# Kernel tuning notes

Hardware: AMD Instinct MI355X
Metric: run time of the kernel (lower is better)

The kernel has to match this reference:

```python
import jax, jax.numpy as jnp
import numpy as np

ESP = 1e-10  # matches SRKNN.ESP
K = 16       # top-k neighbors


def _logmap(x):
    # sign-preserving log map (repo helper not shown; eps matches SRKNN.ESP)
    return jnp.sign(x) * jnp.log(jnp.abs(x) + ESP)


def setup_inputs() -> dict:
    key = jax.random.key(0)
    k1, k2, k3, k4 = jax.random.split(key, 4)
    B, C, H, W = 2, 128, 32, 32
    C2 = C // 2
    X = jax.random.normal(k1, (B, C, H, W), jnp.float32)
    # nn.Linear(C, C//2, bias=False) weights, torch layout [out, in]
    W_min = jax.random.normal(k2, (C2, C), jnp.float32) * 0.08
    W_sub = jax.random.normal(k3, (C2, C), jnp.float32) * 0.08
    M = jax.random.normal(k4, (C2, C2), jnp.float32)
    return {"X": X, "W_min": W_min, "W_sub": W_sub, "M": M}


def reference(X, W_min, W_sub, M):
    B, C, H, W = X.shape
    XV = jnp.transpose(X, (0, 2, 3, 1)).reshape(B, -1, C)  # [B, N, C]
    N = XV.shape[1]
    # project then log-map; pairwise (i=minuend, j=subtrahend) without repeat
    pm = _logmap(XV @ W_min.T)  # [B, N, C2]
    ps = _logmap(XV @ W_sub.T)  # [B, N, C2]
    subR = jax.nn.sigmoid(pm[:, :, None, :] - ps[:, None, :, :])  # [B, N, N, C2]
    A = M.T @ M  # [C2, C2] learned Mahalanobis metric
    dis = jnp.sqrt(jnp.sum(jnp.einsum('bijc,cd->bijd', subR, A) * subR, axis=-1))  # [B,N,N]
    diff = jax.nn.sigmoid(-dis)
    value, index = jax.lax.top_k(diff, K)  # [B, N, K]
    value = -value.reshape(B, -1, 1)       # [B, N*K, 1]
    index = index.reshape(B, -1)           # [B, N*K]
    return index, value
```

## Files before the change

### kernel.cpp

```cpp
#include <hip/hip_runtime.h>
#include <hip/hip_bf16.h>
#include <hip/hip_fp16.h>
#include <math.h>

#define NN 1024
#define CC 128
#define C2 64
#define KK 16
#define NCAND 24

#if __has_builtin(__builtin_amdgcn_exp2f)
#define EXP2F(x) __builtin_amdgcn_exp2f(x)
#else
#define EXP2F(x) exp2f(x)
#endif
#define LOG2E 1.4426950408889634f

typedef __fp16  hf2   __attribute__((ext_vector_type(2)));
typedef _Float16 half8 __attribute__((ext_vector_type(8)));
typedef float f32x4    __attribute__((ext_vector_type(4)));
typedef int   int4v    __attribute__((ext_vector_type(4)));
typedef unsigned int uint;

__device__ __forceinline__ float fast_rcp(float x) {
    return __builtin_amdgcn_rcpf(x);
}

#define LDS_FENCE() do { \
    asm volatile("s_waitcnt lgkmcnt(0)" ::: "memory"); \
    __builtin_amdgcn_sched_barrier(0); } while (0)

__global__ __launch_bounds__(128) void proj_buildA(
        const float* __restrict__ X,
        const float* __restrict__ Wm,
        const float* __restrict__ Ws,
        const float* __restrict__ M,
        float* __restrict__ pm,
        float* __restrict__ ps,
        float* __restrict__ psE,
        float* __restrict__ A) {
    if (blockIdx.x >= 2 * NN) {
        const int e = (blockIdx.x - 2 * NN) * 128 + threadIdx.x;
        const int c = e >> 6, d = e & 63;
        float acc = 0.f;
        #pragma unroll 8
        for (int r = 0; r < C2; ++r)
            acc = fmaf(M[r * C2 + c], M[r * C2 + d], acc);
        A[e] = acc;
        return;
    }

    const int bn = blockIdx.x;
    const int b  = bn >> 10;
    const int n  = bn & (NN - 1);
    const int t  = threadIdx.x;

    __shared__ float xv[CC];
    xv[t] = X[b * CC * NN + t * NN + n];
    __syncthreads();

    const int d = t & (C2 - 1);
    const float* wr = ((t < C2) ? Wm : Ws) + d * CC;
    float acc = 0.f;
    #pragma unroll
    for (int c = 0; c < CC; ++c)
        acc = fmaf(wr[c], xv[c], acc);

    float a = __fadd_rn(fabsf(acc), 1e-10f);
    float l = logf(a);
    float r = (acc > 0.f) ? l : ((acc < 0.f) ? -l : 0.f);
    if (t < C2) {
        pm[bn * C2 + d] = r;
    } else {
        ps[bn * C2 + d] = r;
        psE[bn * C2 + d] = EXP2F(r * LOG2E);
    }
}

#define SIGF16(PMEF, Y0, Y1, BF) do {                                         \
    float s0 = PMEF[0] * fast_rcp(PMEF[0] + (Y0).x);                          \
    float s1 = PMEF[1] * fast_rcp(PMEF[1] + (Y0).y);                          \
    float s2 = PMEF[2] * fast_rcp(PMEF[2] + (Y0).z);                          \
    float s3 = PMEF[3] * fast_rcp(PMEF[3] + (Y0).w);                          \
    float s4 = PMEF[4] * fast_rcp(PMEF[4] + (Y1).x);                          \
    float s5 = PMEF[5] * fast_rcp(PMEF[5] + (Y1).y);                          \
    float s6 = PMEF[6] * fast_rcp(PMEF[6] + (Y1).z);                          \
    float s7 = PMEF[7] * fast_rcp(PMEF[7] + (Y1).w);                          \
    hf2 p0 = __builtin_amdgcn_cvt_pkrtz(s0, s1);                              \
    hf2 p1 = __builtin_amdgcn_cvt_pkrtz(s2, s3);                              \
    hf2 p2 = __builtin_amdgcn_cvt_pkrtz(s4, s5);                              \
    hf2 p3 = __builtin_amdgcn_cvt_pkrtz(s6, s7);                              \
    int4v iv = { __builtin_bit_cast(int, p0), __builtin_bit_cast(int, p1),    \
                 __builtin_bit_cast(int, p2), __builtin_bit_cast(int, p3) };  \
    BF = __builtin_bit_cast(half8, iv);                                       \
} while (0)

#define MFMA4(AC, KT, B)                                                              \
    AC[0] = __builtin_amdgcn_mfma_f32_16x16x32_f16(af[0][KT], B, AC[0], 0, 0, 0);     \
    AC[1] = __builtin_amdgcn_mfma_f32_16x16x32_f16(af[1][KT], B, AC[1], 0, 0, 0);     \
    AC[2] = __builtin_amdgcn_mfma_f32_16x16x32_f16(af[2][KT], B, AC[2], 0, 0, 0);     \
    AC[3] = __builtin_amdgcn_mfma_f32_16x16x32_f16(af[3][KT], B, AC[3], 0, 0, 0);

#define STREAM(PMEF, T0, T1, T2, T3, AC) do {                                 \
    half8 b0, b1;                                                             \
    SIGF16(PMEF[0], T0, T1, b0);                                              \
    SIGF16(PMEF[1], T2, T3, b1);                                              \
    MFMA4(AC, 0, b0)                                                          \
    MFMA4(AC, 1, b1)                                                          \
} while (0)

__global__ __launch_bounds__(256, 2) void pair_topk(
        const float* __restrict__ pm,
        const float* __restrict__ ps,
        const float* __restrict__ psE,
        const float* __restrict__ Mf,
        const float* __restrict__ A,
        float* __restrict__ out) {
    const int tid  = threadIdx.x;
    const int wv   = tid >> 6;
    const int lane = tid & 63;
    const int g    = lane >> 4;
    const int lj   = lane & 15;
    const int rp   = wv >> 1;
    const int h    = wv & 1;

    const int rbase = blockIdx.x * 4;
    const int b     = rbase >> 10;

    __shared__ uint  d2u[4][NN];
    __shared__ float sC[4][C2];
    __shared__ float cdiffL[4][NCAND];

    const float* psb  = ps  + b * NN * C2;
    const float* psEb = psE + b * NN * C2;

    {
        const int r0 = rbase + rp * 2;

        float pmEf0[2][8], pmEf1[2][8];
        #pragma unroll
        for (int kt = 0; kt < 2; ++kt) {
            const float4 a0 = *(const float4*)(pm + r0 * C2 + kt * 32 + g * 8);
            const float4 a1 = *(const float4*)(pm + r0 * C2 + kt * 32 + g * 8 + 4);
            pmEf0[kt][0] = EXP2F(a0.x * LOG2E); pmEf0[kt][1] = EXP2F(a0.y * LOG2E);
            pmEf0[kt][2] = EXP2F(a0.z * LOG2E); pmEf0[kt][3] = EXP2F(a0.w * LOG2E);
            pmEf0[kt][4] = EXP2F(a1.x * LOG2E); pmEf0[kt][5] = EXP2F(a1.y * LOG2E);
            pmEf0[kt][6] = EXP2F(a1.z * LOG2E); pmEf0[kt][7] = EXP2F(a1.w * LOG2E);
            const float4 c0 = *(const float4*)(pm + (r0 + 1) * C2 + kt * 32 + g * 8);
            const float4 c1 = *(const float4*)(pm + (r0 + 1) * C2 + kt * 32 + g * 8 + 4);
            pmEf1[kt][0] = EXP2F(c0.x * LOG2E); pmEf1[kt][1] = EXP2F(c0.y * LOG2E);
            pmEf1[kt][2] = EXP2F(c0.z * LOG2E); pmEf1[kt][3] = EXP2F(c0.w * LOG2E);
            pmEf1[kt][4] = EXP2F(c1.x * LOG2E); pmEf1[kt][5] = EXP2F(c1.y * LOG2E);
            pmEf1[kt][6] = EXP2F(c1.z * LOG2E); pmEf1[kt][7] = EXP2F(c1.w * LOG2E);
        }

        half8 af[4][2];
        #pragma unroll
        for (int rt = 0; rt < 4; ++rt) {
            #pragma unroll
            for (int kt = 0; kt < 2; ++kt) {
                const float* mrow = Mf + (rt * 16 + lj) * C2 + kt * 32 + g * 8;
                const float4 m0 = *(const float4*)mrow;
                const float4 m1 = *(const float4*)(mrow + 4);
                float mv[8] = {m0.x, m0.y, m0.z, m0.w, m1.x, m1.y, m1.z, m1.w};
                #pragma unroll
                for (int e = 0; e < 8; ++e)
                    af[rt][kt][e] = (_Float16)mv[e];
            }
        }

        const int tbase = h * 32;
        const float* p0 = psEb + (long)((tbase + 0) * 16 + lj) * C2 + g * 8;
        const float* p1 = psEb + (long)((tbase + 1) * 16 + lj) * C2 + g * 8;
        float4 cA0 = *(const float4*)(p0);      float4 cA1 = *(const float4*)(p0 + 4);
        float4 cA2 = *(const float4*)(p0 + 32); float4 cA3 = *(const float4*)(p0 + 36);
        float4 cB0 = *(const float4*)(p1);      float4 cB1 = *(const float4*)(p1 + 4);
        float4 cB2 = *(const float4*)(p1 + 32); float4 cB3 = *(const float4*)(p1 + 36);

        #pragma unroll 1
        for (int it = 0; it < 16; ++it) {
            float4 nA0, nA1, nA2, nA3, nB0, nB1, nB2, nB3;
            if (it < 15) {
                const float* q0 = psEb + (long)((tbase + it * 2 + 2) * 16 + lj) * C2 + g * 8;
                const float* q1 = psEb + (long)((tbase + it * 2 + 3) * 16 + lj) * C2 + g * 8;
                nA0 = *(const float4*)(q0);      nA1 = *(const float4*)(q0 + 4);
                nA2 = *(const float4*)(q0 + 32); nA3 = *(const float4*)(q0 + 36);
                nB0 = *(const float4*)(q1);      nB1 = *(const float4*)(q1 + 4);
                nB2 = *(const float4*)(q1 + 32); nB3 = *(const float4*)(q1 + 36);
            }

            f32x4 a0A[4] = {{0,0,0,0},{0,0,0,0},{0,0,0,0},{0,0,0,0}};
            f32x4 a1A[4] = {{0,0,0,0},{0,0,0,0},{0,0,0,0},{0,0,0,0}};
            f32x4 a0B[4] = {{0,0,0,0},{0,0,0,0},{0,0,0,0},{0,0,0,0}};
            f32x4 a1B[4] = {{0,0,0,0},{0,0,0,0},{0,0,0,0},{0,0,0,0}};

            __builtin_amdgcn_s_setprio(1);
            STREAM(pmEf0, cA0, cA1, cA2, cA3, a0A);
            STREAM(pmEf1, cA0, cA1, cA2, cA3, a1A);
            STREAM(pmEf0, cB0, cB1, cB2, cB3, a0B);
            STREAM(pmEf1, cB0, cB1, cB2, cB3, a1B);
            __builtin_amdgcn_s_setprio(0);

            float s0A = 0.f, s1A = 0.f, s0B = 0.f, s1B = 0.f;
            #pragma unroll
            for (int e = 0; e < 4; ++e) {
                s0A = fmaf(a0A[0][e], a0A[0][e], s0A);
                s0A = fmaf(a0A[1][e], a0A[1][e], s0A);
                s0A = fmaf(a0A[2][e], a0A[2][e], s0A);
                s0A = fmaf(a0A[3][e], a0A[3][e], s0A);
                s1A = fmaf(a1A[0][e], a1A[0][e], s1A);
                s1A = fmaf(a1A[1][e], a1A[1][e], s1A);
                s1A = fmaf(a1A[2][e], a1A[2][e], s1A);
                s1A = fmaf(a1A[3][e], a1A[3][e], s1A);
                s0B = fmaf(a0B[0][e], a0B[0][e], s0B);
                s0B = fmaf(a0B[1][e], a0B[1][e], s0B);
                s0B = fmaf(a0B[2][e], a0B[2][e], s0B);
                s0B = fmaf(a0B[3][e], a0B[3][e], s0B);
                s1B = fmaf(a1B[0][e], a1B[0][e], s1B);
                s1B = fmaf(a1B[1][e], a1B[1][e], s1B);
                s1B = fmaf(a1B[2][e], a1B[2][e], s1B);
                s1B = fmaf(a1B[3][e], a1B[3][e], s1B);
            }
            s0A += __shfl_xor(s0A, 16, 64); s0A += __shfl_xor(s0A, 32, 64);
            s1A += __shfl_xor(s1A, 16, 64); s1A += __shfl_xor(s1A, 32, 64);
            s0B += __shfl_xor(s0B, 16, 64); s0B += __shfl_xor(s0B, 32, 64);
            s1B += __shfl_xor(s1B, 16, 64); s1B += __shfl_xor(s1B, 32, 64);
            if (lane < 16) {
                const int jA = (tbase + it * 2 + 0) * 16 + lane;
                const int jB = (tbase + it * 2 + 1) * 16 + lane;
                d2u[rp * 2 + 0][jA] = (__float_as_uint(s0A) & 0xFFFFFC00u) | (uint)jA;
                d2u[rp * 2 + 1][jA] = (__float_as_uint(s1A) & 0xFFFFFC00u) | (uint)jA;
                d2u[rp * 2 + 0][jB] = (__float_as_uint(s0B) & 0xFFFFFC00u) | (uint)jB;
                d2u[rp * 2 + 1][jB] = (__float_as_uint(s1B) & 0xFFFFFC00u) | (uint)jB;
            }

            cA0 = nA0; cA1 = nA1; cA2 = nA2; cA3 = nA3;
            cB0 = nB0; cB1 = nB1; cB2 = nB2; cB3 = nB3;
        }
    }
    __syncthreads();

    const int bi = rbase + wv;
    const int i  = bi & (NN - 1);
    const float pm_own = pm[bi * C2 + lane];

    uint v[16];
    #pragma unroll
    for (int q = 0; q < 16; ++q) v[q] = d2u[wv][q * 64 + lane];

    int myCand = 0;
    #pragma unroll 1
    for (int k = 0; k < NCAND; ++k) {
        uint bv = v[0];
        #pragma unroll
        for (int q = 1; q < 16; ++q) bv = min(bv, v[q]);
        #pragma unroll
        for (int st = 0; st < 6; ++st)
            bv = min(bv, (uint)__shfl_xor((int)bv, 1 << st, 64));
        #pragma unroll
        for (int q = 0; q < 16; ++q)
            if (v[q] == bv) v[q] = 0xFFFFFFFFu;
        if (lane == k) myCand = (int)(bv & 0x3FFu);
    }

    float Acol[C2];
    #pragma unroll
    for (int c = 0; c < C2; ++c) Acol[c] = A[c * C2 + lane];

    int jvv[NCAND];
    #pragma unroll
    for (int t = 0; t < NCAND; ++t) jvv[t] = __shfl(myCand, t, 64);
    float pscv[NCAND];
    #pragma unroll
    for (int t = 0; t < NCAND; ++t) pscv[t] = psb[(long)jvv[t] * C2 + lane];

    #pragma unroll 1
    for (int t = 0; t < NCAND; ++t) {
        float e = expf(pscv[t] - pm_own);
        float s_own = 1.0f / __fadd_rn(1.0f, e);
        sC[wv][lane] = s_own;
        LDS_FENCE();
        float wd = 0.f;
        #pragma unroll
        for (int c = 0; c < C2; ++c)
            wd = fmaf(sC[wv][c], Acol[c], wd);
        const float t_own = __fmul_rn(wd, s_own);
        float r8 = t_own;
        #pragma unroll
        for (int blk = 1; blk < 8; ++blk)
            r8 = __fadd_rn(r8, __shfl(t_own, (lane & 7) + 8 * blk, 64));
        const float rr0 = __shfl(r8, 0, 64), rr1 = __shfl(r8, 1, 64);
        const float rr2 = __shfl(r8, 2, 64), rr3 = __shfl(r8, 3, 64);
        const float rr4 = __shfl(r8, 4, 64), rr5 = __shfl(r8, 5, 64);
        const float rr6 = __shfl(r8, 6, 64), rr7 = __shfl(r8, 7, 64);
        float dis2 = __fadd_rn(
            __fadd_rn(__fadd_rn(rr0, rr1), __fadd_rn(rr2, rr3)),
            __fadd_rn(__fadd_rn(rr4, rr5), __fadd_rn(rr6, rr7)));
        float disf = sqrtf(dis2);
        float ee = expf(disf);
        float cd = 1.0f / __fadd_rn(1.0f, ee);
        if (lane == 0) cdiffL[wv][t] = cd;
    }
    LDS_FENCE();

    float myd = (lane < NCAND) ? cdiffL[wv][lane] : -2.0f;
    int myj = (lane < NCAND) ? myCand : (1 << 20);

    const int obase = b * (NN * KK) + i * KK;
    const int vbase = 2 * NN * KK + obase;

    #pragma unroll 1
    for (int k = 0; k < KK; ++k) {
        float bd = myd;
        int bj = myj;
        #pragma unroll
        for (int st = 0; st < 6; ++st) {
            int msk = 1 << st;
            float od = __shfl_xor(bd, msk, 64);
            int oj = __shfl_xor(bj, msk, 64);
            bool better = (od > bd) || (od == bd && oj < bj);
            bd = better ? od : bd;
            bj = better ? oj : bj;
        }
        if (myj == bj) myd = -2.0f;
        if (lane == 0) {
            out[obase + k] = (float)bj;
            out[vbase + k] = -bd;
        }
    }
}

extern "C" void kernel_launch(void* const* d_in, const int* in_sizes, int n_in,
                              void* d_out, int out_size, void* d_ws, size_t ws_size,
                              hipStream_t stream) {
    const float* X  = (const float*)d_in[0];
    const float* Wm = (const float*)d_in[1];
    const float* Ws = (const float*)d_in[2];
    const float* M  = (const float*)d_in[3];

    float* A   = (float*)d_ws;
    float* pm  = A + C2 * C2;
    float* ps  = pm + 2 * NN * C2;
    float* psE = ps + 2 * NN * C2;
    float* out = (float*)d_out;

    hipLaunchKernelGGL(proj_buildA, dim3(2 * NN + 32), dim3(128), 0, stream,
                       X, Wm, Ws, M, pm, ps, psE, A);
    hipLaunchKernelGGL(pair_topk, dim3(512), dim3(256), 0, stream,
                       pm, ps, psE, M, A, out);
}
```

Before: 94.58 us.

## Give each wave all four rows over a column quarter; pair candidate refinement

The pairwise distance stage now has each wave cover all four query rows against its own quarter of the columns, instead of two rows across half the columns. Each streamed psE tile is converted with sigmoid once and fed to four row-accumulator sets, which halves global loads per wave. The cost is more exp-transformed pm registers held per wave (4x2x8). Separately, the exact candidate rescoring loop now handles two candidates per iteration with a double-buffered shared slot, halving fences and the serial shuffle chains to expose more ILP.

```diff
diff --git a/kernel.cpp b/kernel.cpp
--- a/kernel.cpp
+++ b/kernel.cpp
@@ -109,6 +109,16 @@
     MFMA4(AC, 1, b1)                                                          \
 } while (0)
 
+#define SQUARE16(AC, S) do {                                                  \
+    _Pragma("unroll")                                                         \
+    for (int e = 0; e < 4; ++e) {                                             \
+        S = fmaf(AC[0][e], AC[0][e], S);                                      \
+        S = fmaf(AC[1][e], AC[1][e], S);                                      \
+        S = fmaf(AC[2][e], AC[2][e], S);                                      \
+        S = fmaf(AC[3][e], AC[3][e], S);                                      \
+    }                                                                         \
+} while (0)
+
 __global__ __launch_bounds__(256, 2) void pair_topk(
         const float* __restrict__ pm,
         const float* __restrict__ ps,
@@ -121,37 +131,30 @@
     const int lane = tid & 63;
     const int g    = lane >> 4;
     const int lj   = lane & 15;
-    const int rp   = wv >> 1;
-    const int h    = wv & 1;
 
     const int rbase = blockIdx.x * 4;
     const int b     = rbase >> 10;
 
     __shared__ uint  d2u[4][NN];
-    __shared__ float sC[4][C2];
+    __shared__ float sC[4][2][C2];
     __shared__ float cdiffL[4][NCAND];
 
     const float* psb  = ps  + b * NN * C2;
     const float* psEb = psE + b * NN * C2;
 
     {
-        const int r0 = rbase + rp * 2;
-
-        float pmEf0[2][8], pmEf1[2][8];
-        #pragma unroll
-        for (int kt = 0; kt < 2; ++kt) {
-            const float4 a0 = *(const float4*)(pm + r0 * C2 + kt * 32 + g * 8);
-            const float4 a1 = *(const float4*)(pm + r0 * C2 + kt * 32 + g * 8 + 4);
-            pmEf0[kt][0] = EXP2F(a0.x * LOG2E); pmEf0[kt][1] = EXP2F(a0.y * LOG2E);
-            pmEf0[kt][2] = EXP2F(a0.z * LOG2E); pmEf0[kt][3] = EXP2F(a0.w * LOG2E);
-            pmEf0[kt][4] = EXP2F(a1.x * LOG2E); pmEf0[kt][5] = EXP2F(a1.y * LOG2E);
-            pmEf0[kt][6] = EXP2F(a1.z * LOG2E); pmEf0[kt][7] = EXP2F(a1.w * LOG2E);
-            const float4 c0 = *(const float4*)(pm + (r0 + 1) * C2 + kt * 32 + g * 8);
-            const float4 c1 = *(const float4*)(pm + (r0 + 1) * C2 + kt * 32 + g * 8 + 4);
-            pmEf1[kt][0] = EXP2F(c0.x * LOG2E); pmEf1[kt][1] = EXP2F(c0.y * LOG2E);
-            pmEf1[kt][2] = EXP2F(c0.z * LOG2E); pmEf1[kt][3] = EXP2F(c0.w * LOG2E);
-            pmEf1[kt][4] = EXP2F(c1.x * LOG2E); pmEf1[kt][5] = EXP2F(c1.y * LOG2E);
-            pmEf1[kt][6] = EXP2F(c1.z * LOG2E); pmEf1[kt][7] = EXP2F(c1.w * LOG2E);
+        float pmEf[4][2][8];
+        #pragma unroll
+        for (int r = 0; r < 4; ++r) {
+            #pragma unroll
+            for (int kt = 0; kt < 2; ++kt) {
+                const float4 a0 = *(const float4*)(pm + (rbase + r) * C2 + kt * 32 + g * 8);
+                const float4 a1 = *(const float4*)(pm + (rbase + r) * C2 + kt * 32 + g * 8 + 4);
+                pmEf[r][kt][0] = EXP2F(a0.x * LOG2E); pmEf[r][kt][1] = EXP2F(a0.y * LOG2E);
+                pmEf[r][kt][2] = EXP2F(a0.z * LOG2E); pmEf[r][kt][3] = EXP2F(a0.w * LOG2E);
+                pmEf[r][kt][4] = EXP2F(a1.x * LOG2E); pmEf[r][kt][5] = EXP2F(a1.y * LOG2E);
+                pmEf[r][kt][6] = EXP2F(a1.z * LOG2E); pmEf[r][kt][7] = EXP2F(a1.w * LOG2E);
+            }
         }
 
         half8 af[4][2];
@@ -169,73 +172,50 @@
             }
         }
 
-        const int tbase = h * 32;
+        const int tbase = wv * 16;
         const float* p0 = psEb + (long)((tbase + 0) * 16 + lj) * C2 + g * 8;
-        const float* p1 = psEb + (long)((tbase + 1) * 16 + lj) * C2 + g * 8;
-        float4 cA0 = *(const float4*)(p0);      float4 cA1 = *(const float4*)(p0 + 4);
-        float4 cA2 = *(const float4*)(p0 + 32); float4 cA3 = *(const float4*)(p0 + 36);
-        float4 cB0 = *(const float4*)(p1);      float4 cB1 = *(const float4*)(p1 + 4);
-        float4 cB2 = *(const float4*)(p1 + 32); float4 cB3 = *(const float4*)(p1 + 36);
+        float4 c0 = *(const float4*)(p0);      float4 c1 = *(const float4*)(p0 + 4);
+        float4 c2 = *(const float4*)(p0 + 32); float4 c3 = *(const float4*)(p0 + 36);
 
         #pragma unroll 1
         for (int it = 0; it < 16; ++it) {
-            float4 nA0, nA1, nA2, nA3, nB0, nB1, nB2, nB3;
+            float4 n0, n1, n2, n3;
             if (it < 15) {
-                const float* q0 = psEb + (long)((tbase + it * 2 + 2) * 16 + lj) * C2 + g * 8;
-                const float* q1 = psEb + (long)((tbase + it * 2 + 3) * 16 + lj) * C2 + g * 8;
-                nA0 = *(const float4*)(q0);      nA1 = *(const float4*)(q0 + 4);
-                nA2 = *(const float4*)(q0 + 32); nA3 = *(const float4*)(q0 + 36);
-                nB0 = *(const float4*)(q1);      nB1 = *(const float4*)(q1 + 4);
-                nB2 = *(const float4*)(q1 + 32); nB3 = *(const float4*)(q1 + 36);
+                const float* q0 = psEb + (long)((tbase + it + 1) * 16 + lj) * C2 + g * 8;
+                n0 = *(const float4*)(q0);      n1 = *(const float4*)(q0 + 4);
+                n2 = *(const float4*)(q0 + 32); n3 = *(const float4*)(q0 + 36);
             }
 
-            f32x4 a0A[4] = {{0,0,0,0},{0,0,0,0},{0,0,0,0},{0,0,0,0}};
-            f32x4 a1A[4] = {{0,0,0,0},{0,0,0,0},{0,0,0,0},{0,0,0,0}};
-            f32x4 a0B[4] = {{0,0,0,0},{0,0,0,0},{0,0,0,0},{0,0,0,0}};
-            f32x4 a1B[4] = {{0,0,0,0},{0,0,0,0},{0,0,0,0},{0,0,0,0}};
+            f32x4 ac0[4] = {{0,0,0,0},{0,0,0,0},{0,0,0,0},{0,0,0,0}};
+            f32x4 ac1[4] = {{0,0,0,0},{0,0,0,0},{0,0,0,0},{0,0,0,0}};
+            f32x4 ac2[4] = {{0,0,0,0},{0,0,0,0},{0,0,0,0},{0,0,0,0}};
+            f32x4 ac3[4] = {{0,0,0,0},{0,0,0,0},{0,0,0,0},{0,0,0,0}};
 
             __builtin_amdgcn_s_setprio(1);
-            STREAM(pmEf0, cA0, cA1, cA2, cA3, a0A);
-            STREAM(pmEf1, cA0, cA1, cA2, cA3, a1A);
-            STREAM(pmEf0, cB0, cB1, cB2, cB3, a0B);
-            STREAM(pmEf1, cB0, cB1, cB2, cB3, a1B);
+            STREAM(pmEf[0], c0, c1, c2, c3, ac0);
+            STREAM(pmEf[1], c0, c1, c2, c3, ac1);
+            STREAM(pmEf[2], c0, c1, c2, c3, ac2);
+            STREAM(pmEf[3], c0, c1, c2, c3, ac3);
             __builtin_amdgcn_s_setprio(0);
 
-            float s0A = 0.f, s1A = 0.f, s0B = 0.f, s1B = 0.f;
-            #pragma unroll
-            for (int e = 0; e < 4; ++e) {
-                s0A = fmaf(a0A[0][e], a0A[0][e], s0A);
-                s0A = fmaf(a0A[1][e], a0A[1][e], s0A);
-                s0A = fmaf(a0A[2][e], a0A[2][e], s0A);
-                s0A = fmaf(a0A[3][e], a0A[3][e], s0A);
-                s1A = fmaf(a1A[0][e], a1A[0][e], s1A);
-                s1A = fmaf(a1A[1][e], a1A[1][e], s1A);
-                s1A = fmaf(a1A[2][e], a1A[2][e], s1A);
-                s1A = fmaf(a1A[3][e], a1A[3][e], s1A);
-                s0B = fmaf(a0B[0][e], a0B[0][e], s0B);
-                s0B = fmaf(a0B[1][e], a0B[1][e], s0B);
-                s0B = fmaf(a0B[2][e], a0B[2][e], s0B);
-                s0B = fmaf(a0B[3][e], a0B[3][e], s0B);
-                s1B = fmaf(a1B[0][e], a1B[0][e], s1B);
-                s1B = fmaf(a1B[1][e], a1B[1][e], s1B);
-                s1B = fmaf(a1B[2][e], a1B[2][e], s1B);
-                s1B = fmaf(a1B[3][e], a1B[3][e], s1B);
+            float s0 = 0.f, s1 = 0.f, s2 = 0.f, s3 = 0.f;
+            SQUARE16(ac0, s0);
+            SQUARE16(ac1, s1);
+            SQUARE16(ac2, s2);
+            SQUARE16(ac3, s3);
+            s0 += __shfl_xor(s0, 16, 64); s0 += __shfl_xor(s0, 32, 64);
+            s1 += __shfl_xor(s1, 16, 64); s1 += __shfl_xor(s1, 32, 64);
+            s2 += __shfl_xor(s2, 16, 64); s2 += __shfl_xor(s2, 32, 64);
+            s3 += __shfl_xor(s3, 16, 64); s3 += __shfl_xor(s3, 32, 64);
+            if (lane < 16) {
+                const int jj = (tbase + it) * 16 + lane;
+                d2u[0][jj] = (__float_as_uint(s0) & 0xFFFFFC00u) | (uint)jj;
+                d2u[1][jj] = (__float_as_uint(s1) & 0xFFFFFC00u) | (uint)jj;
+                d2u[2][jj] = (__float_as_uint(s2) & 0xFFFFFC00u) | (uint)jj;
+                d2u[3][jj] = (__float_as_uint(s3) & 0xFFFFFC00u) | (uint)jj;
             }
-            s0A += __shfl_xor(s0A, 16, 64); s0A += __shfl_xor(s0A, 32, 64);
-            s1A += __shfl_xor(s1A, 16, 64); s1A += __shfl_xor(s1A, 32, 64);
-            s0B += __shfl_xor(s0B, 16, 64); s0B += __shfl_xor(s0B, 32, 64);
-            s1B += __shfl_xor(s1B, 16, 64); s1B += __shfl_xor(s1B, 32, 64);
-            if (lane < 16) {
-                const int jA = (tbase + it * 2 + 0) * 16 + lane;
-                const int jB = (tbase + it * 2 + 1) * 16 + lane;
-                d2u[rp * 2 + 0][jA] = (__float_as_uint(s0A) & 0xFFFFFC00u) | (uint)jA;
-                d2u[rp * 2 + 1][jA] = (__float_as_uint(s1A) & 0xFFFFFC00u) | (uint)jA;
-                d2u[rp * 2 + 0][jB] = (__float_as_uint(s0B) & 0xFFFFFC00u) | (uint)jB;
-                d2u[rp * 2 + 1][jB] = (__float_as_uint(s1B) & 0xFFFFFC00u) | (uint)jB;
-            }
-
-            cA0 = nA0; cA1 = nA1; cA2 = nA2; cA3 = nA3;
-            cB0 = nB0; cB1 = nB1; cB2 = nB2; cB3 = nB3;
+
+            c0 = n0; c1 = n1; c2 = n2; c3 = n3;
         }
     }
     __syncthreads();
@@ -275,31 +255,44 @@
     for (int t = 0; t < NCAND; ++t) pscv[t] = psb[(long)jvv[t] * C2 + lane];
 
     #pragma unroll 1
-    for (int t = 0; t < NCAND; ++t) {
-        float e = expf(pscv[t] - pm_own);
-        float s_own = 1.0f / __fadd_rn(1.0f, e);
-        sC[wv][lane] = s_own;
+    for (int t = 0; t < NCAND; t += 2) {
+        float e0 = expf(pscv[t]     - pm_own);
+        float e1 = expf(pscv[t + 1] - pm_own);
+        float sA = 1.0f / __fadd_rn(1.0f, e0);
+        float sB = 1.0f / __fadd_rn(1.0f, e1);
+        sC[wv][0][lane] = sA;
+        sC[wv][1][lane] = sB;
         LDS_FENCE();
-        float wd = 0.f;
-        #pragma unroll
-        for (int c = 0; c < C2; ++c)
-            wd = fmaf(sC[wv][c], Acol[c], wd);
-        const float t_own = __fmul_rn(wd, s_own);
-        float r8 = t_own;
-        #pragma unroll
-        for (int blk = 1; blk < 8; ++blk)
-            r8 = __fadd_rn(r8, __shfl(t_own, (lane & 7) + 8 * blk, 64));
-        const float rr0 = __shfl(r8, 0, 64), rr1 = __shfl(r8, 1, 64);
-        const float rr2 = __shfl(r8, 2, 64), rr3 = __shfl(r8, 3, 64);
-        const float rr4 = __shfl(r8, 4, 64), rr5 = __shfl(r8, 5, 64);
-        const float rr6 = __shfl(r8, 6, 64), rr7 = __shfl(r8, 7, 64);
-        float dis2 = __fadd_rn(
-            __fadd_rn(__fadd_rn(rr0, rr1), __fadd_rn(rr2, rr3)),
-            __fadd_rn(__fadd_rn(rr4, rr5), __fadd_rn(rr6, rr7)));
-        float disf = sqrtf(dis2);
-        float ee = expf(disf);
-        float cd = 1.0f / __fadd_rn(1.0f, ee);
-        if (lane == 0) cdiffL[wv][t] = cd;
+        float wd0 = 0.f, wd1 = 0.f;
+        #pragma unroll
+        for (int c = 0; c < C2; ++c) {
+            wd0 = fmaf(sC[wv][0][c], Acol[c], wd0);
+            wd1 = fmaf(sC[wv][1][c], Acol[c], wd1);
+        }
+        const float t0 = __fmul_rn(wd0, sA);
+        const float t1 = __fmul_rn(wd1, sB);
+        float r80 = t0, r81 = t1;
+        #pragma unroll
+        for (int blk = 1; blk < 8; ++blk) {
+            r80 = __fadd_rn(r80, __shfl(t0, (lane & 7) + 8 * blk, 64));
+            r81 = __fadd_rn(r81, __shfl(t1, (lane & 7) + 8 * blk, 64));
+        }
+        float dis2a = __fadd_rn(
+            __fadd_rn(__fadd_rn(__shfl(r80, 0, 64), __shfl(r80, 1, 64)),
+                      __fadd_rn(__shfl(r80, 2, 64), __shfl(r80, 3, 64))),
+            __fadd_rn(__fadd_rn(__shfl(r80, 4, 64), __shfl(r80, 5, 64)),
+                      __fadd_rn(__shfl(r80, 6, 64), __shfl(r80, 7, 64))));
+        float dis2b = __fadd_rn(
+            __fadd_rn(__fadd_rn(__shfl(r81, 0, 64), __shfl(r81, 1, 64)),
+                      __fadd_rn(__shfl(r81, 2, 64), __shfl(r81, 3, 64))),
+            __fadd_rn(__fadd_rn(__shfl(r81, 4, 64), __shfl(r81, 5, 64)),
+                      __fadd_rn(__shfl(r81, 6, 64), __shfl(r81, 7, 64))));
+        float cda = 1.0f / __fadd_rn(1.0f, expf(sqrtf(dis2a)));
+        float cdb = 1.0f / __fadd_rn(1.0f, expf(sqrtf(dis2b)));
+        if (lane == 0) {
+            cdiffL[wv][t]     = cda;
+            cdiffL[wv][t + 1] = cdb;
+        }
     }
     LDS_FENCE();
 
```

Result: faster. 88.56 us, median of 2 (-6.4%).
